# Optimization experiments

Hardware: AMD Instinct MI355X
Metric: run time of the kernel (lower is better)

## Reference

```python
import jax, jax.numpy as jnp
import numpy as np

N_NODES = 50000
BN_EPS = 1e-5


def gcn_conv(x, W, b, src, dst, n):
    # PyG GCNConv: add self-loops, symmetric normalization, linear then scatter-add, bias after.
    h = x @ W                                             # [N, out]
    loops = jnp.arange(n, dtype=src.dtype)
    s = jnp.concatenate([src, loops])                     # [E+N]
    d = jnp.concatenate([dst, loops])                     # [E+N]
    deg = jax.ops.segment_sum(jnp.ones_like(d, dtype=h.dtype), d, num_segments=n)
    dinv = jnp.where(deg > 0, jax.lax.rsqrt(deg), 0.0)    # deg^-1/2
    norm = dinv[s] * dinv[d]                              # [E+N]
    msg = h[s] * norm[:, None]                            # gather + scale
    out = jax.ops.segment_sum(msg, d, num_segments=n)     # scatter-add to targets
    return out + b


def batch_norm(x, gamma, beta):
    # training-mode BatchNorm1d: batch stats over node dim, biased variance
    mean = jnp.mean(x, axis=0)
    var = jnp.mean(jnp.square(x - mean), axis=0)
    return (x - mean) * jax.lax.rsqrt(var + BN_EPS) * gamma + beta


def setup_inputs() -> dict:
    key = jax.random.key(0)
    ks = jax.random.split(key, 4)
    n, e = N_NODES, 800000
    c_in, c_hid, c_out = 128, 128, 64
    x = jax.random.normal(ks[0], (n, c_in), dtype=jnp.float32)
    edge_index = jax.random.randint(ks[1], (2, e), 0, n, dtype=jnp.int64)
    W1 = jax.random.normal(ks[2], (c_in, c_hid), dtype=jnp.float32) / np.sqrt(c_in)
    W2 = jax.random.normal(ks[3], (c_hid, c_out), dtype=jnp.float32) / np.sqrt(c_hid)
    return {
        "x": x,
        "edge_index": edge_index,
        "W1": W1,
        "b1": jnp.zeros((c_hid,), jnp.float32),
        "gamma": jnp.ones((c_hid,), jnp.float32),
        "beta": jnp.zeros((c_hid,), jnp.float32),
        "W2": W2,
        "b2": jnp.zeros((c_out,), jnp.float32),
    }


def reference(x, edge_index, W1, b1, gamma, beta, W2, b2):
    src, dst = edge_index[0], edge_index[1]
    n = x.shape[0]
    h = gcn_conv(x, W1, b1, src, dst, n)
    h = batch_norm(h, gamma, beta)
    h = jax.nn.elu(h)
    z = gcn_conv(h, W2, b2, src, dst, n)
    return z
```

## Files before the change

kernel.cpp:

```cpp
#include <hip/hip_runtime.h>
#include <math.h>

#define C_IN 128
#define C_HID 128
#define C_OUT 64
#define BN_EPS 1e-5f
#define CHUNK 1024
#define NBB 96
#define CAP 108192
#define LSTR 67

typedef unsigned int uint;
typedef unsigned short ushort;
typedef int iv4 __attribute__((ext_vector_type(4)));
typedef short bfx8 __attribute__((ext_vector_type(8)));
typedef float fx4 __attribute__((ext_vector_type(4)));

__device__ __forceinline__ uint bfr(float f) {
    uint u = __float_as_uint(f);
    return (u + 0x7fffu + ((u >> 16) & 1u)) >> 16;
}
__device__ __forceinline__ uint pk(float a, float b) { return bfr(a) | (bfr(b) << 16); }
__device__ __forceinline__ float bl(uint u) { return __uint_as_float(u << 16); }
__device__ __forceinline__ float bh(uint u) { return __uint_as_float(u & 0xffff0000u); }

__global__ __launch_bounds__(256) void k_zero(int* __restrict__ deg,
                                              float* __restrict__ gsum,
                                              float* __restrict__ gss,
                                              int* __restrict__ bcur, int n) {
    int i = blockIdx.x * 256 + threadIdx.x;
    if (i < n) deg[i] = 0;
    else if (i < n + 128) gsum[i - n] = 0.f;
    else if (i < n + 256) gss[i - n - 128] = 0.f;
    else if (i < n + 264) bcur[i - n - 256] = 0;
}

__global__ __launch_bounds__(256) void k_bucket(const int* __restrict__ src,
                                                const int* __restrict__ dst,
                                                int* __restrict__ deg,
                                                int* __restrict__ bcur,
                                                int2* __restrict__ stage,
                                                int E, float binv) {
    __shared__ int cnt[8], base[8], off[8];
    if (threadIdx.x < 8) { cnt[threadIdx.x] = 0; off[threadIdx.x] = 0; }
    __syncthreads();
    int e0 = blockIdx.x * CHUNK;
    int e1 = e0 + CHUNK; if (e1 > E) e1 = E;
    int nv = (e1 - e0) & ~3;
    for (int e = e0 + threadIdx.x * 4; e < e0 + nv; e += 1024) {
        iv4 d4 = *(const iv4*)&dst[e];
        #pragma unroll
        for (int j = 0; j < 4; ++j) {
            int d = d4[j];
            atomicAdd(&deg[d], 1);
            int b = (int)((float)d * binv); if (b > 7) b = 7;
            atomicAdd(&cnt[b], 1);
        }
    }
    for (int e = e0 + nv + threadIdx.x; e < e1; e += 256) {
        int d = dst[e];
        atomicAdd(&deg[d], 1);
        int b = (int)((float)d * binv); if (b > 7) b = 7;
        atomicAdd(&cnt[b], 1);
    }
    __syncthreads();
    if (threadIdx.x < 8) base[threadIdx.x] = atomicAdd(&bcur[threadIdx.x], cnt[threadIdx.x]);
    __syncthreads();
    for (int e = e0 + threadIdx.x * 4; e < e0 + nv; e += 1024) {
        iv4 d4 = *(const iv4*)&dst[e];
        iv4 s4 = *(const iv4*)&src[e];
        #pragma unroll
        for (int j = 0; j < 4; ++j) {
            int d = d4[j], s = s4[j];
            int b = (int)((float)d * binv); if (b > 7) b = 7;
            int o = base[b] + atomicAdd(&off[b], 1);
            if (o < CAP) stage[(size_t)b * CAP + o] = make_int2(d, s);
        }
    }
    for (int e = e0 + nv + threadIdx.x; e < e1; e += 256) {
        int d = dst[e], s = src[e];
        int b = (int)((float)d * binv); if (b > 7) b = 7;
        int o = base[b] + atomicAdd(&off[b], 1);
        if (o < CAP) stage[(size_t)b * CAP + o] = make_int2(d, s);
    }
}

__global__ __launch_bounds__(256) void k_part(const int* __restrict__ deg,
                                              int* __restrict__ part, int n) {
    int i = blockIdx.x * 256 + threadIdx.x;
    int v = (i < n) ? deg[i] : 0;
    #pragma unroll
    for (int o = 32; o > 0; o >>= 1) v += __shfl_down(v, o);
    __shared__ int ls[4];
    if ((threadIdx.x & 63) == 0) ls[threadIdx.x >> 6] = v;
    __syncthreads();
    if (threadIdx.x == 0) part[blockIdx.x] = ls[0] + ls[1] + ls[2] + ls[3];
}

__global__ __launch_bounds__(256) void k_scanp(int* __restrict__ part, int nb) {
    __shared__ int s[256];
    int tid = threadIdx.x;
    int v = (tid < nb) ? part[tid] : 0;
    s[tid] = v;
    __syncthreads();
    for (int o = 1; o < 256; o <<= 1) {
        int t = (tid >= o) ? s[tid - o] : 0;
        __syncthreads();
        s[tid] += t;
        __syncthreads();
    }
    if (tid < nb) part[tid] = s[tid] - v;
}

__global__ __launch_bounds__(256) void k_apply(const int* __restrict__ deg,
                                               const int* __restrict__ part,
                                               int* __restrict__ rowstart,
                                               int* __restrict__ cursor,
                                               float* __restrict__ dinv, int n) {
    int i = blockIdx.x * 256 + threadIdx.x;
    int d = (i < n) ? deg[i] : 0;
    __shared__ int s[256];
    s[threadIdx.x] = d;
    __syncthreads();
    for (int o = 1; o < 256; o <<= 1) {
        int t = (threadIdx.x >= o) ? s[threadIdx.x - o] : 0;
        __syncthreads();
        s[threadIdx.x] += t;
        __syncthreads();
    }
    int incl = s[threadIdx.x];
    int off = part[blockIdx.x];
    if (i < n) {
        rowstart[i] = off + incl - d;
        cursor[i]   = off + incl - d;
        dinv[i] = rsqrtf((float)(d + 1));
        if (i == n - 1) rowstart[n] = off + incl;
    }
}

__global__ __launch_bounds__(256) void k_fill2(const int2* __restrict__ stage,
                                               const int* __restrict__ bcur,
                                               int* __restrict__ cursor,
                                               int* __restrict__ csr) {
    int b = blockIdx.x & 7;
    int j = blockIdx.x >> 3;
    int cnt = bcur[b]; if (cnt > CAP) cnt = CAP;
    const int2* sp = stage + (size_t)b * CAP;
    for (int i = j * 256 + threadIdx.x; i < cnt; i += NBB * 256) {
        int2 pr = sp[i];
        csr[atomicAdd(&cursor[pr.x], 1)] = pr.y;
    }
}

__global__ __launch_bounds__(256) void k_gemm1(const float* __restrict__ x,
                                               const float* __restrict__ W,
                                               ushort* __restrict__ h, int n) {
    __shared__ uint xsp[64 * LSTR];
    __shared__ uint wtp[128 * LSTR];
    const int tid = threadIdx.x;
    const int w = tid >> 6, l = tid & 63;
    const int lo = l & 15, hi = l >> 4;
    const int base = blockIdx.x * 64;

    for (int idx = tid; idx < 64 * 32; idx += 256) {
        int row = idx >> 5, c4 = (idx & 31) * 4;
        float4 v = make_float4(0.f, 0.f, 0.f, 0.f);
        if (base + row < n) v = *(const float4*)&x[(size_t)(base + row) * C_IN + c4];
        xsp[row * LSTR + (c4 >> 1)]     = pk(v.x, v.y);
        xsp[row * LSTR + (c4 >> 1) + 1] = pk(v.z, v.w);
    }
    for (int idx = tid; idx < 64 * 32; idx += 256) {
        int kk = idx >> 5, n4 = (idx & 31) * 4;
        float4 w0 = *(const float4*)&W[(size_t)(2 * kk) * C_HID + n4];
        float4 w1 = *(const float4*)&W[(size_t)(2 * kk + 1) * C_HID + n4];
        wtp[(n4 + 0) * LSTR + kk] = pk(w0.x, w1.x);
        wtp[(n4 + 1) * LSTR + kk] = pk(w0.y, w1.y);
        wtp[(n4 + 2) * LSTR + kk] = pk(w0.z, w1.z);
        wtp[(n4 + 3) * LSTR + kk] = pk(w0.w, w1.w);
    }
    __syncthreads();

    fx4 acc[8];
    #pragma unroll
    for (int t = 0; t < 8; ++t) acc[t] = (fx4)(0.f);

    const int arow = (w * 16 + lo) * LSTR;
    #pragma unroll
    for (int kb = 0; kb < 4; ++kb) {
        const int ka = kb * 16 + hi * 4;
        uint4 ua;
        ua.x = xsp[arow + ka]; ua.y = xsp[arow + ka + 1];
        ua.z = xsp[arow + ka + 2]; ua.w = xsp[arow + ka + 3];
        bfx8 af = __builtin_bit_cast(bfx8, ua);
        #pragma unroll
        for (int nt = 0; nt < 8; ++nt) {
            const int brow = (nt * 16 + lo) * LSTR;
            uint4 ub;
            ub.x = wtp[brow + ka]; ub.y = wtp[brow + ka + 1];
            ub.z = wtp[brow + ka + 2]; ub.w = wtp[brow + ka + 3];
            bfx8 bf_ = __builtin_bit_cast(bfx8, ub);
            acc[nt] = __builtin_amdgcn_mfma_f32_16x16x32_bf16(af, bf_, acc[nt], 0, 0, 0);
        }
    }
    #pragma unroll
    for (int nt = 0; nt < 8; ++nt) {
        #pragma unroll
        for (int r = 0; r < 4; ++r) {
            int row = base + w * 16 + hi * 4 + r;
            if (row < n) h[(size_t)row * C_HID + nt * 16 + lo] = (ushort)bfr(acc[nt][r]);
        }
    }
}

__global__ __launch_bounds__(256) void k_gather1(const uint4* __restrict__ h,
                                                 const float* __restrict__ dinv,
                                                 const int* __restrict__ rowstart,
                                                 const int* __restrict__ csr,
                                                 const float* __restrict__ b,
                                                 uint4* __restrict__ g1, int n) {
    int v = (blockIdx.x * 256 + threadIdx.x) >> 4;
    int l = threadIdx.x & 15;
    if (v >= n) return;
    float dv = dinv[v];
    int s0 = rowstart[v], s1 = rowstart[v + 1];
    float4 aA, aB;
    {
        uint4 u = h[(size_t)v * 16 + l];
        aA.x = dv * bl(u.x); aA.y = dv * bh(u.x); aA.z = dv * bl(u.y); aA.w = dv * bh(u.y);
        aB.x = dv * bl(u.z); aB.y = dv * bh(u.z); aB.z = dv * bl(u.w); aB.w = dv * bh(u.w);
    }
    int e = s0;
    for (; e + 3 < s1; e += 4) {
        int i0 = csr[e], i1 = csr[e + 1], i2 = csr[e + 2], i3 = csr[e + 3];
        float w0 = dinv[i0], w1 = dinv[i1], w2 = dinv[i2], w3 = dinv[i3];
        uint4 u0 = h[(size_t)i0 * 16 + l];
        uint4 u1 = h[(size_t)i1 * 16 + l];
        uint4 u2 = h[(size_t)i2 * 16 + l];
        uint4 u3 = h[(size_t)i3 * 16 + l];
        aA.x += w0 * bl(u0.x) + w1 * bl(u1.x) + w2 * bl(u2.x) + w3 * bl(u3.x);
        aA.y += w0 * bh(u0.x) + w1 * bh(u1.x) + w2 * bh(u2.x) + w3 * bh(u3.x);
        aA.z += w0 * bl(u0.y) + w1 * bl(u1.y) + w2 * bl(u2.y) + w3 * bl(u3.y);
        aA.w += w0 * bh(u0.y) + w1 * bh(u1.y) + w2 * bh(u2.y) + w3 * bh(u3.y);
        aB.x += w0 * bl(u0.z) + w1 * bl(u1.z) + w2 * bl(u2.z) + w3 * bl(u3.z);
        aB.y += w0 * bh(u0.z) + w1 * bh(u1.z) + w2 * bh(u2.z) + w3 * bh(u3.z);
        aB.z += w0 * bl(u0.w) + w1 * bl(u1.w) + w2 * bl(u2.w) + w3 * bl(u3.w);
        aB.w += w0 * bh(u0.w) + w1 * bh(u1.w) + w2 * bh(u2.w) + w3 * bh(u3.w);
    }
    for (; e < s1; ++e) {
        int s = csr[e];
        float w = dinv[s];
        uint4 u = h[(size_t)s * 16 + l];
        aA.x += w * bl(u.x); aA.y += w * bh(u.x); aA.z += w * bl(u.y); aA.w += w * bh(u.y);
        aB.x += w * bl(u.z); aB.y += w * bh(u.z); aB.z += w * bl(u.w); aB.w += w * bh(u.w);
    }
    float4 b0 = *(const float4*)&b[l * 8];
    float4 b1v = *(const float4*)&b[l * 8 + 4];
    uint4 o;
    o.x = pk(aA.x * dv + b0.x,  aA.y * dv + b0.y);
    o.y = pk(aA.z * dv + b0.z,  aA.w * dv + b0.w);
    o.z = pk(aB.x * dv + b1v.x, aB.y * dv + b1v.y);
    o.w = pk(aB.z * dv + b1v.z, aB.w * dv + b1v.w);
    g1[(size_t)v * 16 + l] = o;
}

__global__ __launch_bounds__(256) void k_bnstats(const uint4* __restrict__ g,
                                                 float* __restrict__ gsum,
                                                 float* __restrict__ gss, int n) {
    float4 sA = make_float4(0.f,0.f,0.f,0.f), sB = sA, qA = sA, qB = sA;
    int total = n * 16;
    int stride = gridDim.x * 256;
    for (int i = blockIdx.x * 256 + threadIdx.x; i < total; i += stride) {
        uint4 u = g[i];
        float v0 = bl(u.x), v1 = bh(u.x), v2 = bl(u.y), v3 = bh(u.y);
        float v4 = bl(u.z), v5 = bh(u.z), v6 = bl(u.w), v7 = bh(u.w);
        sA.x += v0; sA.y += v1; sA.z += v2; sA.w += v3;
        sB.x += v4; sB.y += v5; sB.z += v6; sB.w += v7;
        qA.x += v0*v0; qA.y += v1*v1; qA.z += v2*v2; qA.w += v3*v3;
        qB.x += v4*v4; qB.y += v5*v5; qB.z += v6*v6; qB.w += v7*v7;
    }
    __shared__ float sb[128], qb[128];
    if (threadIdx.x < 128) { sb[threadIdx.x] = 0.f; qb[threadIdx.x] = 0.f; }
    __syncthreads();
    int c0 = (threadIdx.x & 15) * 8;
    atomicAdd(&sb[c0+0], sA.x); atomicAdd(&sb[c0+1], sA.y); atomicAdd(&sb[c0+2], sA.z); atomicAdd(&sb[c0+3], sA.w);
    atomicAdd(&sb[c0+4], sB.x); atomicAdd(&sb[c0+5], sB.y); atomicAdd(&sb[c0+6], sB.z); atomicAdd(&sb[c0+7], sB.w);
    atomicAdd(&qb[c0+0], qA.x); atomicAdd(&qb[c0+1], qA.y); atomicAdd(&qb[c0+2], qA.z); atomicAdd(&qb[c0+3], qA.w);
    atomicAdd(&qb[c0+4], qB.x); atomicAdd(&qb[c0+5], qB.y); atomicAdd(&qb[c0+6], qB.z); atomicAdd(&qb[c0+7], qB.w);
    __syncthreads();
    if (threadIdx.x < 128) {
        atomicAdd(&gsum[threadIdx.x], sb[threadIdx.x]);
        atomicAdd(&gss[threadIdx.x], qb[threadIdx.x]);
    }
}

__global__ __launch_bounds__(256) void k_gemm2(const uint4* __restrict__ g1,
                                               const float* __restrict__ W2,
                                               const float* __restrict__ gsum,
                                               const float* __restrict__ gss,
                                               const float* __restrict__ gamma,
                                               const float* __restrict__ beta,
                                               ushort* __restrict__ h2, int n) {
    __shared__ uint xsp[64 * LSTR];
    __shared__ uint wtp[64 * LSTR];
    __shared__ float sc[C_HID], sh[C_HID];
    const int tid = threadIdx.x;
    const int w = tid >> 6, l = tid & 63;
    const int lo = l & 15, hi = l >> 4;
    const int base = blockIdx.x * 64;

    if (tid < C_HID) {
        float inv_n = 1.f / (float)n;
        float mean = gsum[tid] * inv_n;
        float var = gss[tid] * inv_n - mean * mean;
        float s = gamma[tid] * rsqrtf(var + BN_EPS);
        sc[tid] = s;
        sh[tid] = beta[tid] - mean * s;
    }
    __syncthreads();

    for (int idx = tid; idx < 64 * 16; idx += 256) {
        int row = idx >> 4, q = idx & 15;
        int k8 = q * 8;
        uint4 u = make_uint4(0, 0, 0, 0);
        if (base + row < n) u = g1[(size_t)(base + row) * 16 + q];
        float t;
        float e0, e1, e2, e3, e4, e5, e6, e7;
        t = bl(u.x) * sc[k8+0] + sh[k8+0]; e0 = t > 0.f ? t : expm1f(t);
        t = bh(u.x) * sc[k8+1] + sh[k8+1]; e1 = t > 0.f ? t : expm1f(t);
        t = bl(u.y) * sc[k8+2] + sh[k8+2]; e2 = t > 0.f ? t : expm1f(t);
        t = bh(u.y) * sc[k8+3] + sh[k8+3]; e3 = t > 0.f ? t : expm1f(t);
        t = bl(u.z) * sc[k8+4] + sh[k8+4]; e4 = t > 0.f ? t : expm1f(t);
        t = bh(u.z) * sc[k8+5] + sh[k8+5]; e5 = t > 0.f ? t : expm1f(t);
        t = bl(u.w) * sc[k8+6] + sh[k8+6]; e6 = t > 0.f ? t : expm1f(t);
        t = bh(u.w) * sc[k8+7] + sh[k8+7]; e7 = t > 0.f ? t : expm1f(t);
        int wbase = row * LSTR + q * 4;
        xsp[wbase + 0] = pk(e0, e1);
        xsp[wbase + 1] = pk(e2, e3);
        xsp[wbase + 2] = pk(e4, e5);
        xsp[wbase + 3] = pk(e6, e7);
    }
    for (int idx = tid; idx < 64 * 16; idx += 256) {
        int kk = idx >> 4, n4 = (idx & 15) * 4;
        float4 w0 = *(const float4*)&W2[(size_t)(2 * kk) * C_OUT + n4];
        float4 w1 = *(const float4*)&W2[(size_t)(2 * kk + 1) * C_OUT + n4];
        wtp[(n4 + 0) * LSTR + kk] = pk(w0.x, w1.x);
        wtp[(n4 + 1) * LSTR + kk] = pk(w0.y, w1.y);
        wtp[(n4 + 2) * LSTR + kk] = pk(w0.z, w1.z);
        wtp[(n4 + 3) * LSTR + kk] = pk(w0.w, w1.w);
    }
    __syncthreads();

    fx4 acc[4];
    #pragma unroll
    for (int t = 0; t < 4; ++t) acc[t] = (fx4)(0.f);

    const int arow = (w * 16 + lo) * LSTR;
    #pragma unroll
    for (int kb = 0; kb < 4; ++kb) {
        const int ka = kb * 16 + hi * 4;
        uint4 ua;
        ua.x = xsp[arow + ka]; ua.y = xsp[arow + ka + 1];
        ua.z = xsp[arow + ka + 2]; ua.w = xsp[arow + ka + 3];
        bfx8 af = __builtin_bit_cast(bfx8, ua);
        #pragma unroll
        for (int nt = 0; nt < 4; ++nt) {
            const int brow = (nt * 16 + lo) * LSTR;
            uint4 ub;
            ub.x = wtp[brow + ka]; ub.y = wtp[brow + ka + 1];
            ub.z = wtp[brow + ka + 2]; ub.w = wtp[brow + ka + 3];
            bfx8 bf_ = __builtin_bit_cast(bfx8, ub);
            acc[nt] = __builtin_amdgcn_mfma_f32_16x16x32_bf16(af, bf_, acc[nt], 0, 0, 0);
        }
    }
    #pragma unroll
    for (int nt = 0; nt < 4; ++nt) {
        #pragma unroll
        for (int r = 0; r < 4; ++r) {
            int row = base + w * 16 + hi * 4 + r;
            if (row < n) h2[(size_t)row * C_OUT + nt * 16 + lo] = (ushort)bfr(acc[nt][r]);
        }
    }
}

__global__ __launch_bounds__(256) void k_gather2(const uint2* __restrict__ h,
                                                 const float* __restrict__ dinv,
                                                 const int* __restrict__ rowstart,
                                                 const int* __restrict__ csr,
                                                 const float* __restrict__ b,
                                                 float* __restrict__ out, int n) {
    int v = (blockIdx.x * 256 + threadIdx.x) >> 4;
    int l = threadIdx.x & 15;
    if (v >= n) return;
    float dv = dinv[v];
    int s0 = rowstart[v], s1 = rowstart[v + 1];
    float4 a;
    {
        uint2 u = h[(size_t)v * 16 + l];
        a.x = dv * bl(u.x); a.y = dv * bh(u.x); a.z = dv * bl(u.y); a.w = dv * bh(u.y);
    }
    int e = s0;
    for (; e + 3 < s1; e += 4) {
        int i0 = csr[e], i1 = csr[e + 1], i2 = csr[e + 2], i3 = csr[e + 3];
        float w0 = dinv[i0], w1 = dinv[i1], w2 = dinv[i2], w3 = dinv[i3];
        uint2 u0 = h[(size_t)i0 * 16 + l];
        uint2 u1 = h[(size_t)i1 * 16 + l];
        uint2 u2 = h[(size_t)i2 * 16 + l];
        uint2 u3 = h[(size_t)i3 * 16 + l];
        a.x += w0 * bl(u0.x) + w1 * bl(u1.x) + w2 * bl(u2.x) + w3 * bl(u3.x);
        a.y += w0 * bh(u0.x) + w1 * bh(u1.x) + w2 * bh(u2.x) + w3 * bh(u3.x);
        a.z += w0 * bl(u0.y) + w1 * bl(u1.y) + w2 * bl(u2.y) + w3 * bl(u3.y);
        a.w += w0 * bh(u0.y) + w1 * bh(u1.y) + w2 * bh(u2.y) + w3 * bh(u3.y);
    }
    for (; e < s1; ++e) {
        int s = csr[e];
        float w = dinv[s];
        uint2 u = h[(size_t)s * 16 + l];
        a.x += w * bl(u.x); a.y += w * bh(u.x); a.z += w * bl(u.y); a.w += w * bh(u.y);
    }
    float4 bb = *(const float4*)&b[l * 4];
    float4 o;
    o.x = a.x * dv + bb.x; o.y = a.y * dv + bb.y;
    o.z = a.z * dv + bb.z; o.w = a.w * dv + bb.w;
    *(float4*)&out[(size_t)v * C_OUT + l * 4] = o;
}

extern "C" void kernel_launch(void* const* d_in, const int* in_sizes, int n_in,
                              void* d_out, int out_size, void* d_ws, size_t ws_size,
                              hipStream_t stream) {
    const float* x     = (const float*)d_in[0];
    const int*   ei    = (const int*)d_in[1];
    const float* W1    = (const float*)d_in[2];
    const float* b1    = (const float*)d_in[3];
    const float* gamma = (const float*)d_in[4];
    const float* beta  = (const float*)d_in[5];
    const float* W2    = (const float*)d_in[6];
    const float* b2    = (const float*)d_in[7];
    float* out = (float*)d_out;

    const int n = in_sizes[0] / C_IN;
    const int E = in_sizes[1] / 2;
    const int* src = ei;
    const int* dst = ei + E;

    char* p = (char*)d_ws;
    auto carve = [&](size_t bytes) {
        char* r = p;
        p += (bytes + 255) & ~(size_t)255;
        return r;
    };
    int*    deg      = (int*)   carve((size_t)n * 4);
    int*    rowstart = (int*)   carve((size_t)(n + 1) * 4);
    int*    cursor   = (int*)   carve((size_t)n * 4);
    int*    csr      = (int*)   carve((size_t)E * 4);
    float*  dinv     = (float*) carve((size_t)n * 4);
    ushort* h1       = (ushort*)carve((size_t)n * 128 * 2);
    ushort* g1       = (ushort*)carve((size_t)n * 128 * 2);
    ushort* h2       = (ushort*)carve((size_t)n * 64 * 2);
    float*  gsum     = (float*) carve(C_HID * 4);
    float*  gss      = (float*) carve(C_HID * 4);
    int*    part     = (int*)   carve(256 * 4);
    int*    bcur     = (int*)   carve(8 * 4);
    int2*   stage    = (int2*)  carve((size_t)8 * CAP * 8);

    const int nb = (n + 255) / 256;
    const int gblocks = (n * 16 + 255) / 256;
    const int fc = (E + CHUNK - 1) / CHUNK;
    const float binv = 8.0f / (float)n;

    k_zero<<<(n + 264 + 255) / 256, 256, 0, stream>>>(deg, gsum, gss, bcur, n);
    k_bucket<<<fc, 256, 0, stream>>>(src, dst, deg, bcur, stage, E, binv);
    k_gemm1<<<(n + 63) / 64, 256, 0, stream>>>(x, W1, h1, n);
    k_part<<<nb, 256, 0, stream>>>(deg, part, n);
    k_scanp<<<1, 256, 0, stream>>>(part, nb);
    k_apply<<<nb, 256, 0, stream>>>(deg, part, rowstart, cursor, dinv, n);
    k_fill2<<<8 * NBB, 256, 0, stream>>>(stage, bcur, cursor, csr);
    k_gather1<<<gblocks, 256, 0, stream>>>((const uint4*)h1, dinv, rowstart, csr, b1, (uint4*)g1, n);
    k_bnstats<<<512, 256, 0, stream>>>((const uint4*)g1, gsum, gss, n);
    k_gemm2<<<(n + 63) / 64, 256, 0, stream>>>((const uint4*)g1, W2, gsum, gss, gamma, beta, h2, n);
    k_gather2<<<gblocks, 256, 0, stream>>>((const uint2*)h2, dinv, rowstart, csr, b2, out, n);
}
```

Before: 192.3 us.

## Fuse BN statistics into first gather and merge partition scan into apply

```diff
diff --git a/kernel.cpp b/kernel.cpp
--- a/kernel.cpp
+++ b/kernel.cpp
@@ -9,6 +9,7 @@
 #define NBB 96
 #define CAP 108192
 #define LSTR 67
+#define G1B 782
 
 typedef unsigned int uint;
 typedef unsigned short ushort;
@@ -97,11 +98,24 @@
     if (threadIdx.x == 0) part[blockIdx.x] = ls[0] + ls[1] + ls[2] + ls[3];
 }
 
-__global__ __launch_bounds__(256) void k_scanp(int* __restrict__ part, int nb) {
+__global__ __launch_bounds__(256) void k_apply(const int* __restrict__ deg,
+                                               const int* __restrict__ part,
+                                               int* __restrict__ rowstart,
+                                               int* __restrict__ cursor,
+                                               float* __restrict__ dinv, int n, int nb) {
+    const int tid = threadIdx.x;
+    int pv = (tid < blockIdx.x && tid < nb) ? part[tid] : 0;
+    #pragma unroll
+    for (int o = 32; o > 0; o >>= 1) pv += __shfl_down(pv, o);
+    __shared__ int ws[4];
+    if ((tid & 63) == 0) ws[tid >> 6] = pv;
+    __syncthreads();
+    int off = ws[0] + ws[1] + ws[2] + ws[3];
+
+    int i = blockIdx.x * 256 + tid;
+    int d = (i < n) ? deg[i] : 0;
     __shared__ int s[256];
-    int tid = threadIdx.x;
-    int v = (tid < nb) ? part[tid] : 0;
-    s[tid] = v;
+    s[tid] = d;
     __syncthreads();
     for (int o = 1; o < 256; o <<= 1) {
         int t = (tid >= o) ? s[tid - o] : 0;
@@ -109,27 +123,7 @@
         s[tid] += t;
         __syncthreads();
     }
-    if (tid < nb) part[tid] = s[tid] - v;
-}
-
-__global__ __launch_bounds__(256) void k_apply(const int* __restrict__ deg,
-                                               const int* __restrict__ part,
-                                               int* __restrict__ rowstart,
-                                               int* __restrict__ cursor,
-                                               float* __restrict__ dinv, int n) {
-    int i = blockIdx.x * 256 + threadIdx.x;
-    int d = (i < n) ? deg[i] : 0;
-    __shared__ int s[256];
-    s[threadIdx.x] = d;
-    __syncthreads();
-    for (int o = 1; o < 256; o <<= 1) {
-        int t = (threadIdx.x >= o) ? s[threadIdx.x - o] : 0;
-        __syncthreads();
-        s[threadIdx.x] += t;
-        __syncthreads();
-    }
-    int incl = s[threadIdx.x];
-    int off = part[blockIdx.x];
+    int incl = s[tid];
     if (i < n) {
         rowstart[i] = off + incl - d;
         cursor[i]   = off + incl - d;
@@ -217,79 +211,78 @@
                                                  const int* __restrict__ rowstart,
                                                  const int* __restrict__ csr,
                                                  const float* __restrict__ b,
-                                                 uint4* __restrict__ g1, int n) {
-    int v = (blockIdx.x * 256 + threadIdx.x) >> 4;
-    int l = threadIdx.x & 15;
-    if (v >= n) return;
-    float dv = dinv[v];
-    int s0 = rowstart[v], s1 = rowstart[v + 1];
-    float4 aA, aB;
-    {
-        uint4 u = h[(size_t)v * 16 + l];
-        aA.x = dv * bl(u.x); aA.y = dv * bh(u.x); aA.z = dv * bl(u.y); aA.w = dv * bh(u.y);
-        aB.x = dv * bl(u.z); aB.y = dv * bh(u.z); aB.z = dv * bl(u.w); aB.w = dv * bh(u.w);
-    }
-    int e = s0;
-    for (; e + 3 < s1; e += 4) {
-        int i0 = csr[e], i1 = csr[e + 1], i2 = csr[e + 2], i3 = csr[e + 3];
-        float w0 = dinv[i0], w1 = dinv[i1], w2 = dinv[i2], w3 = dinv[i3];
-        uint4 u0 = h[(size_t)i0 * 16 + l];
-        uint4 u1 = h[(size_t)i1 * 16 + l];
-        uint4 u2 = h[(size_t)i2 * 16 + l];
-        uint4 u3 = h[(size_t)i3 * 16 + l];
-        aA.x += w0 * bl(u0.x) + w1 * bl(u1.x) + w2 * bl(u2.x) + w3 * bl(u3.x);
-        aA.y += w0 * bh(u0.x) + w1 * bh(u1.x) + w2 * bh(u2.x) + w3 * bh(u3.x);
-        aA.z += w0 * bl(u0.y) + w1 * bl(u1.y) + w2 * bl(u2.y) + w3 * bl(u3.y);
-        aA.w += w0 * bh(u0.y) + w1 * bh(u1.y) + w2 * bh(u2.y) + w3 * bh(u3.y);
-        aB.x += w0 * bl(u0.z) + w1 * bl(u1.z) + w2 * bl(u2.z) + w3 * bl(u3.z);
-        aB.y += w0 * bh(u0.z) + w1 * bh(u1.z) + w2 * bh(u2.z) + w3 * bh(u3.z);
-        aB.z += w0 * bl(u0.w) + w1 * bl(u1.w) + w2 * bl(u2.w) + w3 * bl(u3.w);
-        aB.w += w0 * bh(u0.w) + w1 * bh(u1.w) + w2 * bh(u2.w) + w3 * bh(u3.w);
-    }
-    for (; e < s1; ++e) {
-        int s = csr[e];
-        float w = dinv[s];
-        uint4 u = h[(size_t)s * 16 + l];
-        aA.x += w * bl(u.x); aA.y += w * bh(u.x); aA.z += w * bl(u.y); aA.w += w * bh(u.y);
-        aB.x += w * bl(u.z); aB.y += w * bh(u.z); aB.z += w * bl(u.w); aB.w += w * bh(u.w);
-    }
+                                                 uint4* __restrict__ g1,
+                                                 float* __restrict__ gsum,
+                                                 float* __restrict__ gss, int n) {
+    const int tid = threadIdx.x;
+    const int l = tid & 15;
+    const int gid = (blockIdx.x * 256 + tid) >> 4;
+    const int ngr = gridDim.x * 16;
+
     float4 b0 = *(const float4*)&b[l * 8];
     float4 b1v = *(const float4*)&b[l * 8 + 4];
-    uint4 o;
-    o.x = pk(aA.x * dv + b0.x,  aA.y * dv + b0.y);
-    o.y = pk(aA.z * dv + b0.z,  aA.w * dv + b0.w);
-    o.z = pk(aB.x * dv + b1v.x, aB.y * dv + b1v.y);
-    o.w = pk(aB.z * dv + b1v.z, aB.w * dv + b1v.w);
-    g1[(size_t)v * 16 + l] = o;
-}
-
-__global__ __launch_bounds__(256) void k_bnstats(const uint4* __restrict__ g,
-                                                 float* __restrict__ gsum,
-                                                 float* __restrict__ gss, int n) {
-    float4 sA = make_float4(0.f,0.f,0.f,0.f), sB = sA, qA = sA, qB = sA;
-    int total = n * 16;
-    int stride = gridDim.x * 256;
-    for (int i = blockIdx.x * 256 + threadIdx.x; i < total; i += stride) {
-        uint4 u = g[i];
-        float v0 = bl(u.x), v1 = bh(u.x), v2 = bl(u.y), v3 = bh(u.y);
-        float v4 = bl(u.z), v5 = bh(u.z), v6 = bl(u.w), v7 = bh(u.w);
-        sA.x += v0; sA.y += v1; sA.z += v2; sA.w += v3;
-        sB.x += v4; sB.y += v5; sB.z += v6; sB.w += v7;
-        qA.x += v0*v0; qA.y += v1*v1; qA.z += v2*v2; qA.w += v3*v3;
-        qB.x += v4*v4; qB.y += v5*v5; qB.z += v6*v6; qB.w += v7*v7;
-    }
+
+    float s0=0.f,s1=0.f,s2=0.f,s3=0.f,s4=0.f,s5=0.f,s6=0.f,s7=0.f;
+    float q0=0.f,q1=0.f,q2=0.f,q3=0.f,q4=0.f,q5=0.f,q6=0.f,q7=0.f;
+
+    for (int v = gid; v < n; v += ngr) {
+        float dv = dinv[v];
+        int e0 = rowstart[v], e1 = rowstart[v + 1];
+        float4 aA, aB;
+        {
+            uint4 u = h[(size_t)v * 16 + l];
+            aA.x = dv * bl(u.x); aA.y = dv * bh(u.x); aA.z = dv * bl(u.y); aA.w = dv * bh(u.y);
+            aB.x = dv * bl(u.z); aB.y = dv * bh(u.z); aB.z = dv * bl(u.w); aB.w = dv * bh(u.w);
+        }
+        int e = e0;
+        for (; e + 3 < e1; e += 4) {
+            int i0 = csr[e], i1 = csr[e + 1], i2 = csr[e + 2], i3 = csr[e + 3];
+            float w0 = dinv[i0], w1 = dinv[i1], w2 = dinv[i2], w3 = dinv[i3];
+            uint4 u0 = h[(size_t)i0 * 16 + l];
+            uint4 u1 = h[(size_t)i1 * 16 + l];
+            uint4 u2 = h[(size_t)i2 * 16 + l];
+            uint4 u3 = h[(size_t)i3 * 16 + l];
+            aA.x += w0 * bl(u0.x) + w1 * bl(u1.x) + w2 * bl(u2.x) + w3 * bl(u3.x);
+            aA.y += w0 * bh(u0.x) + w1 * bh(u1.x) + w2 * bh(u2.x) + w3 * bh(u3.x);
+            aA.z += w0 * bl(u0.y) + w1 * bl(u1.y) + w2 * bl(u2.y) + w3 * bl(u3.y);
+            aA.w += w0 * bh(u0.y) + w1 * bh(u1.y) + w2 * bh(u2.y) + w3 * bh(u3.y);
+            aB.x += w0 * bl(u0.z) + w1 * bl(u1.z) + w2 * bl(u2.z) + w3 * bl(u3.z);
+            aB.y += w0 * bh(u0.z) + w1 * bh(u1.z) + w2 * bh(u2.z) + w3 * bh(u3.z);
+            aB.z += w0 * bl(u0.w) + w1 * bl(u1.w) + w2 * bl(u2.w) + w3 * bl(u3.w);
+            aB.w += w0 * bh(u0.w) + w1 * bh(u1.w) + w2 * bh(u2.w) + w3 * bh(u3.w);
+        }
+        for (; e < e1; ++e) {
+            int s = csr[e];
+            float w = dinv[s];
+            uint4 u = h[(size_t)s * 16 + l];
+            aA.x += w * bl(u.x); aA.y += w * bh(u.x); aA.z += w * bl(u.y); aA.w += w * bh(u.y);
+            aB.x += w * bl(u.z); aB.y += w * bh(u.z); aB.z += w * bl(u.w); aB.w += w * bh(u.w);
+        }
+        uint4 o;
+        o.x = pk(aA.x * dv + b0.x,  aA.y * dv + b0.y);
+        o.y = pk(aA.z * dv + b0.z,  aA.w * dv + b0.w);
+        o.z = pk(aB.x * dv + b1v.x, aB.y * dv + b1v.y);
+        o.w = pk(aB.z * dv + b1v.z, aB.w * dv + b1v.w);
+        g1[(size_t)v * 16 + l] = o;
+        float r0 = bl(o.x), r1 = bh(o.x), r2 = bl(o.y), r3 = bh(o.y);
+        float r4 = bl(o.z), r5 = bh(o.z), r6 = bl(o.w), r7 = bh(o.w);
+        s0 += r0; s1 += r1; s2 += r2; s3 += r3; s4 += r4; s5 += r5; s6 += r6; s7 += r7;
+        q0 += r0*r0; q1 += r1*r1; q2 += r2*r2; q3 += r3*r3;
+        q4 += r4*r4; q5 += r5*r5; q6 += r6*r6; q7 += r7*r7;
+    }
+
     __shared__ float sb[128], qb[128];
-    if (threadIdx.x < 128) { sb[threadIdx.x] = 0.f; qb[threadIdx.x] = 0.f; }
-    __syncthreads();
-    int c0 = (threadIdx.x & 15) * 8;
-    atomicAdd(&sb[c0+0], sA.x); atomicAdd(&sb[c0+1], sA.y); atomicAdd(&sb[c0+2], sA.z); atomicAdd(&sb[c0+3], sA.w);
-    atomicAdd(&sb[c0+4], sB.x); atomicAdd(&sb[c0+5], sB.y); atomicAdd(&sb[c0+6], sB.z); atomicAdd(&sb[c0+7], sB.w);
-    atomicAdd(&qb[c0+0], qA.x); atomicAdd(&qb[c0+1], qA.y); atomicAdd(&qb[c0+2], qA.z); atomicAdd(&qb[c0+3], qA.w);
-    atomicAdd(&qb[c0+4], qB.x); atomicAdd(&qb[c0+5], qB.y); atomicAdd(&qb[c0+6], qB.z); atomicAdd(&qb[c0+7], qB.w);
-    __syncthreads();
-    if (threadIdx.x < 128) {
-        atomicAdd(&gsum[threadIdx.x], sb[threadIdx.x]);
-        atomicAdd(&gss[threadIdx.x], qb[threadIdx.x]);
+    if (tid < 128) { sb[tid] = 0.f; qb[tid] = 0.f; }
+    __syncthreads();
+    int c0 = l * 8;
+    atomicAdd(&sb[c0+0], s0); atomicAdd(&sb[c0+1], s1); atomicAdd(&sb[c0+2], s2); atomicAdd(&sb[c0+3], s3);
+    atomicAdd(&sb[c0+4], s4); atomicAdd(&sb[c0+5], s5); atomicAdd(&sb[c0+6], s6); atomicAdd(&sb[c0+7], s7);
+    atomicAdd(&qb[c0+0], q0); atomicAdd(&qb[c0+1], q1); atomicAdd(&qb[c0+2], q2); atomicAdd(&qb[c0+3], q3);
+    atomicAdd(&qb[c0+4], q4); atomicAdd(&qb[c0+5], q5); atomicAdd(&qb[c0+6], q6); atomicAdd(&qb[c0+7], q7);
+    __syncthreads();
+    if (tid < 128) {
+        atomicAdd(&gsum[tid], sb[tid]);
+        atomicAdd(&gss[tid], qb[tid]);
     }
 }
 
@@ -463,7 +456,7 @@
     int2*   stage    = (int2*)  carve((size_t)8 * CAP * 8);
 
     const int nb = (n + 255) / 256;
-    const int gblocks = (n * 16 + 255) / 256;
+    const int g2blocks = (n * 16 + 255) / 256;
     const int fc = (E + CHUNK - 1) / CHUNK;
     const float binv = 8.0f / (float)n;
 
@@ -471,11 +464,10 @@
     k_bucket<<<fc, 256, 0, stream>>>(src, dst, deg, bcur, stage, E, binv);
     k_gemm1<<<(n + 63) / 64, 256, 0, stream>>>(x, W1, h1, n);
     k_part<<<nb, 256, 0, stream>>>(deg, part, n);
-    k_scanp<<<1, 256, 0, stream>>>(part, nb);
-    k_apply<<<nb, 256, 0, stream>>>(deg, part, rowstart, cursor, dinv, n);
+    k_apply<<<nb, 256, 0, stream>>>(deg, part, rowstart, cursor, dinv, n, nb);
     k_fill2<<<8 * NBB, 256, 0, stream>>>(stage, bcur, cursor, csr);
-    k_gather1<<<gblocks, 256, 0, stream>>>((const uint4*)h1, dinv, rowstart, csr, b1, (uint4*)g1, n);
-    k_bnstats<<<512, 256, 0, stream>>>((const uint4*)g1, gsum, gss, n);
+    k_gather1<<<G1B, 256, 0, stream>>>((const uint4*)h1, dinv, rowstart, csr, b1,
+                                       (uint4*)g1, gsum, gss, n);
     k_gemm2<<<(n + 63) / 64, 256, 0, stream>>>((const uint4*)g1, W2, gsum, gss, gamma, beta, h2, n);
-    k_gather2<<<gblocks, 256, 0, stream>>>((const uint2*)h2, dinv, rowstart, csr, b2, out, n);
-}
+    k_gather2<<<g2blocks, 256, 0, stream>>>((const uint2*)h2, dinv, rowstart, csr, b2, out, n);
+}
```

Result: no change. 195.9 us (+1.8%).
